# Kernel optimization log

Measured on AMD Instinct MI355X. Metric: run time of the kernel, lower is better.

## Reference

```python
import jax, jax.numpy as jnp
import numpy as np

B, N, DIN, DH, L = 4, 2048, 128, 128, 4  # batch, n_node, input_dim, hidden_dim, total GAT layers (2 blocks x 2)
NEG = -9.0e15
BN_EPS = 1e-5


def setup_inputs() -> dict:
    key = jax.random.key(0)
    ks = jax.random.split(key, 6)
    x = jax.random.normal(ks[0], (B, N, DIN), jnp.float32)
    adj = jnp.full((N, N), 1.0 / N, jnp.float32)  # nn.Parameter init in GAT.__init__
    stdv1 = 1.0 / np.sqrt(DIN)
    W1 = jax.random.uniform(ks[1], (L, DH, DIN), jnp.float32, -stdv1, stdv1)
    b1 = jax.random.uniform(ks[2], (L, DH), jnp.float32, -stdv1, stdv1)
    stdv2 = 1.0 / np.sqrt(2 * DH)
    a_src = jax.random.uniform(ks[3], (L, DH), jnp.float32, -stdv2, stdv2)
    a_dst = jax.random.uniform(ks[4], (L, DH), jnp.float32, -stdv2, stdv2)
    a_b = jax.random.uniform(ks[5], (L,), jnp.float32, -stdv2, stdv2)
    bn_gamma = jnp.ones((N,), jnp.float32)
    bn_beta = jnp.zeros((N,), jnp.float32)
    bn_mean = jnp.zeros((N,), jnp.float32)
    bn_var = jnp.ones((N,), jnp.float32)
    return {"x": x, "adj": adj, "W1": W1, "b1": b1, "a_src": a_src,
            "a_dst": a_dst, "a_b": a_b, "bn_gamma": bn_gamma, "bn_beta": bn_beta,
            "bn_mean": bn_mean, "bn_var": bn_var}


def _gat_layer(x, mask, W, b, asrc, adst, ab):
    # linear1
    h = jnp.einsum('bnd,fd->bnf', x, W) + b              # [B,N,DH]
    # linear2(cat(h_i, h_j)) == h_i@asrc + h_j@adst + ab  (same math, no O(N^2*2F) tensor)
    s = h @ asrc                                          # [B,N] source term (row i)
    d = h @ adst                                          # [B,N] dest term (col j)
    e = jax.nn.relu(s[:, :, None] + d[:, None, :] + ab)   # [B,N,N]
    att = jnp.where(mask, e, NEG)
    att = jax.nn.softmax(att, axis=2)
    return jnp.einsum('bij,bjf->bif', att, h)


def reference(x, adj, W1, b1, a_src, a_dst, a_b, bn_gamma, bn_beta, bn_mean, bn_var):
    n = x.shape[1]
    eye = jnp.eye(n, dtype=bool)
    A = adj * (1.0 - jnp.eye(n, dtype=adj.dtype))  # self.adj * self.adj_mask (zero diagonal)
    Amask = A > 0

    def block(h, k):
        o1 = _gat_layer(h, Amask, W1[k], b1[k], a_src[k], a_dst[k], a_b[k])
        o2 = _gat_layer(h, eye, W1[k + 1], b1[k + 1], a_src[k + 1], a_dst[k + 1], a_b[k + 1])
        return o1 + o2

    # dropout is inactive in eval mode
    h = jax.nn.relu(block(x, 0))
    # BatchNorm1d(n_node), eval mode: normalize node axis with running stats
    inv = jax.lax.rsqrt(bn_var + BN_EPS)
    h = (h - bn_mean[None, :, None]) * (inv * bn_gamma)[None, :, None] + bn_beta[None, :, None]
    h = block(h, 2)
    return h
```

## Files before the change

kernel.cpp:

```cpp
#include <hip/hip_runtime.h>
#include <math.h>


#define NB 4
#define NN 2048
#define DD 128
#define BNEPS 1e-5f

typedef __attribute__((ext_vector_type(8))) short short8;
typedef __attribute__((ext_vector_type(4))) float f32x4;

__device__ __forceinline__ unsigned short f2bf(float x) {
  unsigned u = __float_as_uint(x);
  u += 0x7fffu + ((u >> 16) & 1u);
  return (unsigned short)(u >> 16);
}
__device__ __forceinline__ unsigned short f2bf_hw(float x) {
  union { __bf16 b; unsigned short u; } cv;
  cv.b = (__bf16)x;
  return cv.u;
}
__device__ __forceinline__ float bf2f(unsigned short h) {
  return __uint_as_float(((unsigned)h) << 16);
}

__global__ __launch_bounds__(256) void k_gemm(
    const float* __restrict__ X, const float* __restrict__ W,
    const float* __restrict__ bias, const float* __restrict__ asrc,
    const float* __restrict__ adst,
    unsigned short* __restrict__ Habf, unsigned short* __restrict__ HaT,
    float* __restrict__ Hb,
    float* __restrict__ SvP0, float* __restrict__ SvP1,
    float* __restrict__ TvP0, float* __restrict__ TvP1,
    float* __restrict__ TotP)
{
  const int layer = blockIdx.x >> 8;
  const int rt    = (blockIdx.x >> 1) & 127;
  const int chf   = blockIdx.x & 1;
  const int row0  = rt * 64;
  const int c0    = chf * 64;
  const float* Wl = W + (size_t)layer * DD * DD;
  const float* bl = bias + layer * DD;

  __shared__ __align__(16) float Xs[32 * 68];
  __shared__ __align__(16) float Ws[32 * 68];
  const int tid = threadIdx.x, tx = tid & 15, ty = tid >> 4;

  float acc[4][4];
#pragma unroll
  for (int i = 0; i < 4; ++i)
#pragma unroll
    for (int j = 0; j < 4; ++j) acc[i][j] = 0.f;

  for (int k0 = 0; k0 < DD; k0 += 32) {
#pragma unroll
    for (int it = 0; it < 2; ++it) {
      const int task = tid + it * 256;
      const int kk = task & 31, rq = task >> 5;
      const float* xb = &X[(size_t)(row0 + rq * 4) * DD + k0 + kk];
      float4 sx;
      sx.x = xb[0]; sx.y = xb[DD]; sx.z = xb[2 * DD]; sx.w = xb[3 * DD];
      *(float4*)&Xs[kk * 68 + rq * 4] = sx;
      const float* wb = &Wl[(size_t)(c0 + rq * 4) * DD + k0 + kk];
      float4 sw_;
      sw_.x = wb[0]; sw_.y = wb[DD]; sw_.z = wb[2 * DD]; sw_.w = wb[3 * DD];
      *(float4*)&Ws[kk * 68 + rq * 4] = sw_;
    }
    __syncthreads();
#pragma unroll
    for (int kk = 0; kk < 32; ++kk) {
      const float4 a = *(const float4*)&Xs[kk * 68 + ty * 4];
      const float4 b = *(const float4*)&Ws[kk * 68 + tx * 4];
      const float av[4] = {a.x, a.y, a.z, a.w};
      const float bv[4] = {b.x, b.y, b.z, b.w};
#pragma unroll
      for (int i = 0; i < 4; ++i)
#pragma unroll
        for (int j = 0; j < 4; ++j)
          acc[i][j] = fmaf(av[i], bv[j], acc[i][j]);
    }
    __syncthreads();
  }

  const int cc = c0 + tx * 4;
  const float4 blv = *(const float4*)&bl[cc];

  if (layer == 1) {
#pragma unroll
    for (int i = 0; i < 4; ++i) {
      const int r = row0 + ty * 4 + i;
      float4 ov;
      ov.x = acc[i][0] + blv.x; ov.y = acc[i][1] + blv.y;
      ov.z = acc[i][2] + blv.z; ov.w = acc[i][3] + blv.w;
      *(float4*)&Hb[(size_t)r * DD + cc] = ov;
    }
    return;
  }

  float avx[4], dvx[4];
#pragma unroll
  for (int j = 0; j < 4; ++j) { avx[j] = asrc[cc + j]; dvx[j] = adst[cc + j]; }
  float sdot[4] = {0.f, 0.f, 0.f, 0.f};
  float tdot[4] = {0.f, 0.f, 0.f, 0.f};
  float tpart[4] = {0.f, 0.f, 0.f, 0.f};
  unsigned short ush[4][4];

#pragma unroll
  for (int i = 0; i < 4; ++i) {
    const int r = row0 + ty * 4 + i;
    float ov[4];
    ov[0] = acc[i][0] + blv.x; ov[1] = acc[i][1] + blv.y;
    ov[2] = acc[i][2] + blv.z; ov[3] = acc[i][3] + blv.w;
#pragma unroll
    for (int j = 0; j < 4; ++j) {
      ush[i][j] = f2bf(ov[j]);
      sdot[i] = fmaf(ov[j], avx[j], sdot[i]);
      tdot[i] = fmaf(ov[j], dvx[j], tdot[i]);
      tpart[j] += ov[j];
    }
    ushort4 hv;
    hv.x = ush[i][0]; hv.y = ush[i][1]; hv.z = ush[i][2]; hv.w = ush[i][3];
    *(ushort4*)&Habf[(size_t)r * DD + cc] = hv;
  }
  {
    const int b   = row0 >> 11;
    const int j0  = (row0 & (NN - 1)) + ty * 4;
    const int cix = j0 >> 5;
    const int q   = (j0 >> 3) & 3;
    const int t   = j0 & 7;
    unsigned short* hp = HaT + (size_t)(b * 64 + cix) * 4096 + q * 8 + t;
#pragma unroll
    for (int j = 0; j < 4; ++j) {
      ushort4 tv;
      tv.x = ush[0][j]; tv.y = ush[1][j]; tv.z = ush[2][j]; tv.w = ush[3][j];
      *(ushort4*)&hp[(size_t)(cc + j) * 32] = tv;
    }
  }
#pragma unroll
  for (int off = 8; off > 0; off >>= 1)
#pragma unroll
    for (int i = 0; i < 4; ++i) {
      sdot[i] += __shfl_xor(sdot[i], off, 64);
      tdot[i] += __shfl_xor(tdot[i], off, 64);
    }
  float* Sp = chf ? SvP1 : SvP0;
  float* Tp = chf ? TvP1 : TvP0;
  if (tx == 0) {
#pragma unroll
    for (int i = 0; i < 4; ++i) {
      const int r = row0 + ty * 4 + i;
      Sp[r] = sdot[i];
      Tp[r] = tdot[i];
    }
  }
  {
    float* redT = Xs;
#pragma unroll
    for (int j = 0; j < 4; ++j) redT[ty * 68 + tx * 4 + j] = tpart[j];
    __syncthreads();
    if (tid < 64) {
      float s = 0.f;
#pragma unroll
      for (int k = 0; k < 16; ++k) s += redT[k * 68 + tid];
      const int b = row0 >> 11, rb = (row0 & (NN - 1)) >> 6;
      TotP[((size_t)(b * 32 + rb)) * DD + c0 + tid] = s;
    }
  }
}

__global__ __launch_bounds__(1024, 4) void k_att(
    const unsigned short* __restrict__ HaT, const unsigned short* __restrict__ Habf,
    const float* __restrict__ Hb,
    const float* __restrict__ SvP0, const float* __restrict__ SvP1,
    const float* __restrict__ TvP0, const float* __restrict__ TvP1,
    const float* __restrict__ ab, const float* __restrict__ TotP,
    const float* __restrict__ gamma, const float* __restrict__ beta,
    const float* __restrict__ mean, const float* __restrict__ var,
    float* __restrict__ Out, int doBN)
{
  const int b  = blockIdx.x >> 6;
  const int i0 = (blockIdx.x & 63) * 32;
  const int tid = threadIdx.x;
  const int wv = tid >> 6, lane = tid & 63, quad = lane >> 4, n = lane & 15;
  const int fq = wv & 3, cq = wv >> 2;

  __shared__ float etl[NN];
  __shared__ float s_blk[32];
  __shared__ float den_sh[32];
  __shared__ float tot_sh[DD];
  __shared__ __align__(16) f32x4 red[54 * 64];

  const float abv = ab[0];
  for (int r = tid; r < NN; r += 1024)
    etl[r] = expf(TvP0[b * NN + r] + TvP1[b * NN + r] + abv);
  if (tid < 32)
    s_blk[tid] = SvP0[b * NN + i0 + tid] + SvP1[b * NN + i0 + tid];
  if (tid < DD) {
    float s = 0.f;
    const float* tp = &TotP[(size_t)b * 32 * DD + tid];
#pragma unroll
    for (int k = 0; k < 32; ++k) s += tp[(size_t)k * DD];
    tot_sh[tid] = s;
  }
  __syncthreads();

  const float es0 = expf(s_blk[n]);
  const float es1 = expf(s_blk[16 + n]);

  f32x4 acc00 = (f32x4){0.f,0.f,0.f,0.f};
  f32x4 acc01 = (f32x4){0.f,0.f,0.f,0.f};
  f32x4 acc10 = (f32x4){0.f,0.f,0.f,0.f};
  f32x4 acc11 = (f32x4){0.f,0.f,0.f,0.f};
  f32x4 accD  = (f32x4){0.f,0.f,0.f,0.f};
  short8 onesb;
#pragma unroll
  for (int j = 0; j < 8; ++j) onesb[j] = (n == 0) ? (short)0x3F80 : (short)0;

  const unsigned short* bb =
      HaT + (size_t)(b * 64 + cq * 16) * 4096 + (fq * 32 + n) * 32 + quad * 8;

  short8 cb0 = *(const short8*)bb;
  short8 cb1 = *(const short8*)(bb + 512);

  for (int cl = 0; cl < 16; ++cl) {
    short8 nb0 = cb0, nb1 = cb1;
    if (cl < 15) {
      const unsigned short* np = bb + (size_t)(cl + 1) * 4096;
      nb0 = *(const short8*)np;
      nb1 = *(const short8*)(np + 512);
    }
    const int jb = (cq * 16 + cl) * 32 + quad * 8;
    const f32x4 ta = *(const f32x4*)&etl[jb];
    const f32x4 tb = *(const f32x4*)&etl[jb + 4];
    const float et[8] = {ta[0], ta[1], ta[2], ta[3], tb[0], tb[1], tb[2], tb[3]};

    short8 a0, a1;
#pragma unroll
    for (int j = 0; j < 8; ++j) {
      a0[j] = (short)f2bf_hw(fmaxf(fmaf(es0, et[j], -1.f), 0.f));
      a1[j] = (short)f2bf_hw(fmaxf(fmaf(es1, et[j], -1.f), 0.f));
    }
    acc00 = __builtin_amdgcn_mfma_f32_16x16x32_bf16(a0, cb0, acc00, 0, 0, 0);
    acc01 = __builtin_amdgcn_mfma_f32_16x16x32_bf16(a0, cb1, acc01, 0, 0, 0);
    acc10 = __builtin_amdgcn_mfma_f32_16x16x32_bf16(a1, cb0, acc10, 0, 0, 0);
    acc11 = __builtin_amdgcn_mfma_f32_16x16x32_bf16(a1, cb1, acc11, 0, 0, 0);
    if (fq == 0)
      accD = __builtin_amdgcn_mfma_f32_16x16x32_bf16(a0, onesb, accD, 0, 0, 0);
    else if (fq == 1)
      accD = __builtin_amdgcn_mfma_f32_16x16x32_bf16(a1, onesb, accD, 0, 0, 0);
    cb0 = nb0;
    cb1 = nb1;
  }

  if (cq > 0) {
    const int base = ((cq - 1) * 4 + fq) * 4;
    red[(base + 0) * 64 + lane] = acc00;
    red[(base + 1) * 64 + lane] = acc01;
    red[(base + 2) * 64 + lane] = acc10;
    red[(base + 3) * 64 + lane] = acc11;
    if (fq < 2) red[(48 + (cq - 1) * 2 + fq) * 64 + lane] = accD;
  }
  __syncthreads();
  if (cq == 0) {
#pragma unroll
    for (int qq = 0; qq < 3; ++qq) {
      const int base = (qq * 4 + fq) * 4;
      acc00 += red[(base + 0) * 64 + lane];
      acc01 += red[(base + 1) * 64 + lane];
      acc10 += red[(base + 2) * 64 + lane];
      acc11 += red[(base + 3) * 64 + lane];
      if (fq < 2) accD += red[(48 + qq * 2 + fq) * 64 + lane];
    }
    if (fq < 2 && n == 0) {
#pragma unroll
      for (int r = 0; r < 4; ++r) den_sh[fq * 16 + quad * 4 + r] = accD[r];
    }
  }
  __syncthreads();

  if (cq == 0) {
#pragma unroll
    for (int g = 0; g < 2; ++g) {
      const f32x4 accA = g ? acc10 : acc00;
      const f32x4 accB = g ? acc11 : acc01;
#pragma unroll
      for (int r = 0; r < 4; ++r) {
        const int iD = g * 16 + quad * 4 + r;
        const int i  = i0 + iD;
        const int gi = b * NN + i;
        const float esi = expf(s_blk[iD]);
        float aii = fmaxf(fmaf(esi, etl[i], -1.f), 0.f);
        aii = bf2f(f2bf_hw(aii));
        const float pii = aii + 1.f;
        const float inv = 1.f / (den_sh[iD] + (float)NN - pii);
        float bnsc = 0.f, bnm = 0.f, bnb = 0.f;
        if (doBN) {
          bnsc = rsqrtf(var[i] + BNEPS) * gamma[i];
          bnm  = mean[i];
          bnb  = beta[i];
        }
#pragma unroll
        for (int ft = 0; ft < 2; ++ft) {
          const int f = fq * 32 + ft * 16 + n;
          const float tot = tot_sh[f];
          const float hdv = bf2f(Habf[(size_t)gi * DD + f]);
          const float numer = (ft ? accB[r] : accA[r]) + tot - pii * hdv;
          float v = numer * inv + Hb[(size_t)gi * DD + f];
          if (doBN) {
            v = fmaxf(v, 0.f);
            v = (v - bnm) * bnsc + bnb;
          }
          Out[(size_t)gi * DD + f] = v;
        }
      }
    }
  }
}

extern "C" void kernel_launch(void* const* d_in, const int* in_sizes, int n_in,
                              void* d_out, int out_size, void* d_ws, size_t ws_size,
                              hipStream_t stream)
{
  const float* x     = (const float*)d_in[0];
  const float* W1    = (const float*)d_in[2];
  const float* b1    = (const float*)d_in[3];
  const float* asrc  = (const float*)d_in[4];
  const float* adst  = (const float*)d_in[5];
  const float* ab    = (const float*)d_in[6];
  const float* gamma = (const float*)d_in[7];
  const float* beta  = (const float*)d_in[8];
  const float* mean  = (const float*)d_in[9];
  const float* var   = (const float*)d_in[10];
  float* out = (float*)d_out;

  char* ws = (char*)d_ws;
  const size_t SZH = (size_t)NB * NN * DD;
  unsigned short* Habf = (unsigned short*)ws; ws += SZH * 2;
  unsigned short* HaT  = (unsigned short*)ws; ws += SZH * 2;
  float* Hb    = (float*)ws; ws += SZH * 4;
  float* Hbn   = (float*)ws; ws += SZH * 4;
  float* SvP0  = (float*)ws; ws += (size_t)NB * NN * 4;
  float* SvP1  = (float*)ws; ws += (size_t)NB * NN * 4;
  float* TvP0  = (float*)ws; ws += (size_t)NB * NN * 4;
  float* TvP1  = (float*)ws; ws += (size_t)NB * NN * 4;
  float* TotP  = (float*)ws; ws += (size_t)NB * 32 * DD * 4;

  for (int pair = 0; pair < 2; ++pair) {
    const int kl = pair * 2;
    const float* Xin = pair ? Hbn : x;
    float* Odst = pair ? out : Hbn;

    k_gemm<<<512, 256, 0, stream>>>(
        Xin, W1 + (size_t)kl * DD * DD, b1 + kl * DD,
        asrc + kl * DD, adst + kl * DD,
        Habf, HaT, Hb, SvP0, SvP1, TvP0, TvP1, TotP);
    k_att<<<256, 1024, 0, stream>>>(
        HaT, Habf, Hb, SvP0, SvP1, TvP0, TvP1, ab + kl, TotP,
        gamma, beta, mean, var, Odst, pair == 0 ? 1 : 0);
  }
}
```

Baseline: 138.9 us.

## Replace FP32 FMA GEMM with split-bf16 MFMA using swizzled LDS tiles

The linear-projection kernel now loads whole 64x128 X and W tiles into LDS as high/low bf16 pairs in an XOR-swizzled layout. It computes the product with three bf16 MFMA instructions per fragment (hi*hi, hi*lo, lo*hi), which keeps close to fp32 accuracy. Results are staged back through LDS into the old per-thread layout for the existing epilogue. This moves the scalar FMA work onto matrix cores, but uses 64KB of LDS per block and adds conversion work.

```diff
diff --git a/kernel.cpp b/kernel.cpp
--- a/kernel.cpp
+++ b/kernel.cpp
@@ -24,7 +24,7 @@
   return __uint_as_float(((unsigned)h) << 16);
 }
 
-__global__ __launch_bounds__(256) void k_gemm(
+__global__ __launch_bounds__(256, 2) void k_gemm(
     const float* __restrict__ X, const float* __restrict__ W,
     const float* __restrict__ bias, const float* __restrict__ asrc,
     const float* __restrict__ adst,
@@ -39,59 +39,93 @@
   const int chf   = blockIdx.x & 1;
   const int row0  = rt * 64;
   const int c0    = chf * 64;
-  const float* Wl = W + (size_t)layer * DD * DD;
-  const float* bl = bias + layer * DD;
-
-  __shared__ __align__(16) float Xs[32 * 68];
-  __shared__ __align__(16) float Ws[32 * 68];
-  const int tid = threadIdx.x, tx = tid & 15, ty = tid >> 4;
-
-  float acc[4][4];
-#pragma unroll
-  for (int i = 0; i < 4; ++i)
-#pragma unroll
-    for (int j = 0; j < 4; ++j) acc[i][j] = 0.f;
-
-  for (int k0 = 0; k0 < DD; k0 += 32) {
-#pragma unroll
-    for (int it = 0; it < 2; ++it) {
-      const int task = tid + it * 256;
-      const int kk = task & 31, rq = task >> 5;
-      const float* xb = &X[(size_t)(row0 + rq * 4) * DD + k0 + kk];
-      float4 sx;
-      sx.x = xb[0]; sx.y = xb[DD]; sx.z = xb[2 * DD]; sx.w = xb[3 * DD];
-      *(float4*)&Xs[kk * 68 + rq * 4] = sx;
-      const float* wb = &Wl[(size_t)(c0 + rq * 4) * DD + k0 + kk];
-      float4 sw_;
-      sw_.x = wb[0]; sw_.y = wb[DD]; sw_.z = wb[2 * DD]; sw_.w = wb[3 * DD];
-      *(float4*)&Ws[kk * 68 + rq * 4] = sw_;
-    }
-    __syncthreads();
-#pragma unroll
-    for (int kk = 0; kk < 32; ++kk) {
-      const float4 a = *(const float4*)&Xs[kk * 68 + ty * 4];
-      const float4 b = *(const float4*)&Ws[kk * 68 + tx * 4];
-      const float av[4] = {a.x, a.y, a.z, a.w};
-      const float bv[4] = {b.x, b.y, b.z, b.w};
-#pragma unroll
-      for (int i = 0; i < 4; ++i)
-#pragma unroll
-        for (int j = 0; j < 4; ++j)
-          acc[i][j] = fmaf(av[i], bv[j], acc[i][j]);
-    }
-    __syncthreads();
-  }
-
+  const float* Wl_ = W + (size_t)layer * DD * DD;
+  const float* bl  = bias + layer * DD;
+
+  __shared__ __align__(16) char smem[65536];
+  unsigned short* XhS = (unsigned short*)smem;
+  unsigned short* XlS = (unsigned short*)(smem + 16384);
+  unsigned short* WhS = (unsigned short*)(smem + 32768);
+  unsigned short* WlS = (unsigned short*)(smem + 49152);
+
+  const int tid = threadIdx.x;
+
+#pragma unroll
+  for (int it = 0; it < 8; ++it) {
+    const int idx = tid + it * 256;
+    const int r   = idx >> 5;
+    const int g4  = idx & 31;
+    const int ui  = ((r * 128 + g4 * 4)) ^ ((r & 7) << 3);
+
+    const float4 xv = *(const float4*)&X[(size_t)(row0 + r) * DD + g4 * 4];
+    ushort4 xh, xl;
+    xh.x = f2bf_hw(xv.x); xl.x = f2bf_hw(xv.x - bf2f(xh.x));
+    xh.y = f2bf_hw(xv.y); xl.y = f2bf_hw(xv.y - bf2f(xh.y));
+    xh.z = f2bf_hw(xv.z); xl.z = f2bf_hw(xv.z - bf2f(xh.z));
+    xh.w = f2bf_hw(xv.w); xl.w = f2bf_hw(xv.w - bf2f(xh.w));
+    *(ushort4*)&XhS[ui] = xh;
+    *(ushort4*)&XlS[ui] = xl;
+
+    const float4 wv = *(const float4*)&Wl_[(size_t)(c0 + r) * DD + g4 * 4];
+    ushort4 wh, wl;
+    wh.x = f2bf_hw(wv.x); wl.x = f2bf_hw(wv.x - bf2f(wh.x));
+    wh.y = f2bf_hw(wv.y); wl.y = f2bf_hw(wv.y - bf2f(wh.y));
+    wh.z = f2bf_hw(wv.z); wl.z = f2bf_hw(wv.z - bf2f(wh.z));
+    wh.w = f2bf_hw(wv.w); wl.w = f2bf_hw(wv.w - bf2f(wh.w));
+    *(ushort4*)&WhS[ui] = wh;
+    *(ushort4*)&WlS[ui] = wl;
+  }
+  __syncthreads();
+
+  const int wv = tid >> 6, lane = tid & 63, quad = lane >> 4, n = lane & 15;
+  f32x4 acc[4];
+#pragma unroll
+  for (int cf = 0; cf < 4; ++cf) acc[cf] = (f32x4){0.f, 0.f, 0.f, 0.f};
+
+  const int ar = wv * 16 + n;
+#pragma unroll
+  for (int ch = 0; ch < 4; ++ch) {
+    const int aidx = ((ar * 128 + ch * 32 + quad * 8)) ^ ((ar & 7) << 3);
+    const short8 ah = *(const short8*)&XhS[aidx];
+    const short8 al = *(const short8*)&XlS[aidx];
+#pragma unroll
+    for (int cf = 0; cf < 4; ++cf) {
+      const int br = cf * 16 + n;
+      const int bidx = ((br * 128 + ch * 32 + quad * 8)) ^ ((br & 7) << 3);
+      const short8 bh = *(const short8*)&WhS[bidx];
+      const short8 bl = *(const short8*)&WlS[bidx];
+      acc[cf] = __builtin_amdgcn_mfma_f32_16x16x32_bf16(ah, bh, acc[cf], 0, 0, 0);
+      acc[cf] = __builtin_amdgcn_mfma_f32_16x16x32_bf16(ah, bl, acc[cf], 0, 0, 0);
+      acc[cf] = __builtin_amdgcn_mfma_f32_16x16x32_bf16(al, bh, acc[cf], 0, 0, 0);
+    }
+  }
+  __syncthreads();
+
+  float* Cs = (float*)smem;
+#pragma unroll
+  for (int cf = 0; cf < 4; ++cf)
+#pragma unroll
+    for (int r = 0; r < 4; ++r)
+      Cs[(wv * 16 + quad * 4 + r) * 68 + cf * 16 + n] = acc[cf][r];
+  __syncthreads();
+
+  const int tx = tid & 15, ty = tid >> 4;
   const int cc = c0 + tx * 4;
   const float4 blv = *(const float4*)&bl[cc];
+  float accE[4][4];
+#pragma unroll
+  for (int i = 0; i < 4; ++i) {
+    const float4 cv = *(const float4*)&Cs[(ty * 4 + i) * 68 + tx * 4];
+    accE[i][0] = cv.x; accE[i][1] = cv.y; accE[i][2] = cv.z; accE[i][3] = cv.w;
+  }
 
   if (layer == 1) {
 #pragma unroll
     for (int i = 0; i < 4; ++i) {
       const int r = row0 + ty * 4 + i;
       float4 ov;
-      ov.x = acc[i][0] + blv.x; ov.y = acc[i][1] + blv.y;
-      ov.z = acc[i][2] + blv.z; ov.w = acc[i][3] + blv.w;
+      ov.x = accE[i][0] + blv.x; ov.y = accE[i][1] + blv.y;
+      ov.z = accE[i][2] + blv.z; ov.w = accE[i][3] + blv.w;
       *(float4*)&Hb[(size_t)r * DD + cc] = ov;
     }
     return;
@@ -109,8 +143,8 @@
   for (int i = 0; i < 4; ++i) {
     const int r = row0 + ty * 4 + i;
     float ov[4];
-    ov[0] = acc[i][0] + blv.x; ov[1] = acc[i][1] + blv.y;
-    ov[2] = acc[i][2] + blv.z; ov[3] = acc[i][3] + blv.w;
+    ov[0] = accE[i][0] + blv.x; ov[1] = accE[i][1] + blv.y;
+    ov[2] = accE[i][2] + blv.z; ov[3] = accE[i][3] + blv.w;
 #pragma unroll
     for (int j = 0; j < 4; ++j) {
       ush[i][j] = f2bf(ov[j]);
@@ -154,7 +188,7 @@
     }
   }
   {
-    float* redT = Xs;
+    float* redT = (float*)(smem + 32768);
 #pragma unroll
     for (int j = 0; j < 4; ++j) redT[ty * 68 + tx * 4 + j] = tpart[j];
     __syncthreads();
```

Result: faster. 129.2 us (-7.0%).
